# Kernel optimization log

Hardware: AMD Instinct MI355X
Metric: run time of the kernel (lower is better)

The kernel has to match this reference:

```python
import jax, jax.numpy as jnp
import numpy as np

C = 768
H = 12
HD = C // H
SCALE = HD ** -0.5
EPS = 1e-5


def setup_inputs() -> dict:
    key = jax.random.key(0)
    kit = iter(jax.random.split(key, 40))
    r = lambda *s: jax.random.normal(next(kit), s, jnp.float32) * 0.02
    d = dict(
        s_x=jax.random.normal(next(kit), (8, 196, C), jnp.float32),
        t_x=jax.random.normal(next(kit), (8, 1568, C), jnp.float32),
        ln1s_g=jnp.ones(C), ln1s_b=jnp.zeros(C),
        mha_w=r(3 * C, C), mha_b=r(3 * C), mha_ow=r(C, C), mha_ob=r(C),
        ln1t_g=jnp.ones(C), ln1t_b=jnp.zeros(C),
        attn_qkv_w=r(3 * C, C), attn_q_b=r(C), attn_v_b=r(C), attn_pw=r(C, C), attn_pb=r(C),
        lnt2s_g=jnp.ones(C), lnt2s_b=jnp.zeros(C),
        t2s_qw=r(C, C), t2s_qb=r(C), t2s_kvw=r(2 * C, C), t2s_kvb=r(C), t2s_pw=r(C, C), t2s_pb=r(C),
        lns2t_g=jnp.ones(C), lns2t_b=jnp.zeros(C),
        s2t_qw=r(C, C), s2t_qb=r(C), s2t_kvw=r(2 * C, C), s2t_kvb=r(C), s2t_pw=r(C, C), s2t_pb=r(C),
        ln2s_g=jnp.ones(C), ln2s_b=jnp.zeros(C),
        cfc_w=r(4 * C, C), cfc_b=r(4 * C), cproj_w=r(C, 4 * C), cproj_b=r(C),
        ln2t_g=jnp.ones(C), ln2t_b=jnp.zeros(C),
        fc1_w=r(4 * C, C), fc1_b=r(4 * C), fc2_w=r(C, 4 * C), fc2_b=r(C),
    )
    return d


def ln(x, g, b):
    m = x.mean(-1, keepdims=True)
    v = jnp.mean((x - m) ** 2, -1, keepdims=True)
    return (x - m) * jax.lax.rsqrt(v + EPS) * g + b


def heads(x):  # (B, N, C) -> (B, H, N, HD)
    B, N, _ = x.shape
    return x.reshape(B, N, H, HD).transpose(0, 2, 1, 3)


def mhsa(q, k, v):  # (B, H, Nq, HD), (B, H, Nk, HD) -> (B, Nq, C)
    a = jax.nn.softmax(jnp.einsum('bhqd,bhkd->bhqk', q * SCALE, k), axis=-1)
    o = jnp.einsum('bhqk,bhkd->bhqd', a, v)
    B, _, Nq, _ = o.shape
    return o.transpose(0, 2, 1, 3).reshape(B, Nq, C)


def reference(s_x, t_x, ln1s_g, ln1s_b, mha_w, mha_b, mha_ow, mha_ob,
              ln1t_g, ln1t_b, attn_qkv_w, attn_q_b, attn_v_b, attn_pw, attn_pb,
              lnt2s_g, lnt2s_b, t2s_qw, t2s_qb, t2s_kvw, t2s_kvb, t2s_pw, t2s_pb,
              lns2t_g, lns2t_b, s2t_qw, s2t_qb, s2t_kvw, s2t_kvb, s2t_pw, s2t_pb,
              ln2s_g, ln2s_b, cfc_w, cfc_b, cproj_w, cproj_b,
              ln2t_g, ln2t_b, fc1_w, fc1_b, fc2_w, fc2_b):
    # 1) clip self-attention. torch nn.MultiheadAttention (batch_first=False)
    # treats axis 0 of the (B, s_N, C) input as the sequence dim, so we
    # faithfully attend over the batch axis.
    y = ln(s_x, ln1s_g, ln1s_b)
    qkv = y @ mha_w.T + mha_b  # (B, s_N, 3C)
    q, k, v = jnp.split(qkv, 3, axis=-1)
    qt, kt, vt = (a.transpose(1, 0, 2) for a in (q, k, v))  # (s_N, B, C)
    o = mhsa(heads(qt), heads(kt), heads(vt))  # (s_N, B, C)
    o = o @ mha_ow.T + mha_ob
    s_x = s_x + o.transpose(1, 0, 2)

    # 2) video-stream self-attention (qkv_bias=True -> cat(q_b, 0, v_b))
    y = ln(t_x, ln1t_g, ln1t_b)
    qkv_bias = jnp.concatenate([attn_q_b, jnp.zeros_like(attn_v_b), attn_v_b])
    qkv = y @ attn_qkv_w.T + qkv_bias
    q, k, v = jnp.split(qkv, 3, axis=-1)
    o = mhsa(heads(q), heads(k), heads(v))
    t_x = t_x + (o @ attn_pw.T + attn_pb)

    # 3) T2S cross: query from LN(s_x), key/value from (updated, un-normed) t_x
    ys = ln(s_x, lnt2s_g, lnt2s_b)
    q = ys @ t2s_qw.T + t2s_qb
    kv = t_x @ t2s_kvw.T + jnp.concatenate([jnp.zeros_like(t2s_kvb), t2s_kvb])
    k, v = jnp.split(kv, 2, axis=-1)
    o = mhsa(heads(q), heads(k), heads(v))
    s_x = s_x + (o @ t2s_pw.T + t2s_pb)

    # 4) S2T cross: query from LN(t_x), key/value from updated s_x
    yt = ln(t_x, lns2t_g, lns2t_b)
    q = yt @ s2t_qw.T + s2t_qb
    kv = s_x @ s2t_kvw.T + jnp.concatenate([jnp.zeros_like(s2t_kvb), s2t_kvb])
    k, v = jnp.split(kv, 2, axis=-1)
    o = mhsa(heads(q), heads(k), heads(v))
    t_x = t_x + (o @ s2t_pw.T + s2t_pb)

    # 5) clip MLP (QuickGELU)
    y = ln(s_x, ln2s_g, ln2s_b)
    h = y @ cfc_w.T + cfc_b
    h = h * jax.nn.sigmoid(1.702 * h)
    s_x = s_x + (h @ cproj_w.T + cproj_b)

    # 6) video MLP (exact GELU, torch default)
    y = ln(t_x, ln2t_g, ln2t_b)
    h = jax.nn.gelu(y @ fc1_w.T + fc1_b, approximate=False)
    t_x = t_x + (h @ fc2_w.T + fc2_b)
    return (s_x, t_x)
```

## Files before the change

kernel.cpp:

```cpp
#include <hip/hip_runtime.h>
#include <stdint.h>


typedef uint16_t u16;
typedef uint16_t u16x8 __attribute__((ext_vector_type(8)));
typedef uint16_t u16x4 __attribute__((ext_vector_type(4)));
typedef short bf16x8 __attribute__((ext_vector_type(8)));
typedef float f32x4 __attribute__((ext_vector_type(4)));

__device__ __forceinline__ float b2f(u16 u) {
    union { float f; uint32_t i; } x;
    x.i = ((uint32_t)u) << 16;
    return x.f;
}
__device__ __forceinline__ u16 f2b(float f) {
    union { float f; uint32_t i; } x;
    x.f = f;
    uint32_t i = x.i;
    uint32_t r = (i + 0x7FFFu + ((i >> 16) & 1u)) >> 16;
    return (u16)r;
}
__device__ __forceinline__ u16 f2b_trunc(float f) {
    union { float f; uint32_t i; } x;
    x.f = f;
    return (u16)(x.i >> 16);
}

__device__ __forceinline__ void gload16(const u16* g, u16* l) {
    __builtin_amdgcn_global_load_lds(
        (const __attribute__((address_space(1))) uint32_t*)g,
        (__attribute__((address_space(3))) uint32_t*)l, 16, 0, 0);
}

struct CvtAll {
    const float* s[14];
    u16* d[14];
    int cum[15];
};
__global__ __launch_bounds__(256) void cvt_all(CvtAll c) {
    int i = blockIdx.x * 256 + threadIdx.x;
    if (i >= c.cum[14]) return;
    int seg = 0;
    #pragma unroll
    for (int k = 1; k < 14; k++) seg += (i >= c.cum[k]);
    int j = i - c.cum[seg];
    c.d[seg][j] = f2b(c.s[seg][j]);
}

__global__ __launch_bounds__(256) void copy_both(
    const float* __restrict__ a, const float* __restrict__ b,
    float* __restrict__ out, int na, int ntot) {
    int i = blockIdx.x * 256 + threadIdx.x;
    if (i < ntot) out[i] = (i < na) ? a[i] : b[i - na];
}

__global__ __launch_bounds__(256) void build_bias_pool(float* __restrict__ dst,
    const float* mha_b, const float* attn_q_b, const float* attn_v_b,
    const float* mha_ob, const float* attn_pb, const float* t2s_kvb,
    const float* t2s_qb, const float* t2s_pb, const float* s2t_qb,
    const float* s2t_kvb, const float* s2t_pb, const float* cfc_b,
    const float* cproj_b, const float* fc1_b, const float* fc2_b) {
    int i = blockIdx.x * 256 + threadIdx.x;
    float v = 0.f;
    if (i < 2304) v = mha_b[i];
    else if (i < 4608) { int j = i - 2304; v = (j < 768) ? attn_q_b[j] : (j < 1536 ? 0.f : attn_v_b[j - 1536]); }
    else if (i < 5376) v = mha_ob[i - 4608];
    else if (i < 6144) v = attn_pb[i - 5376];
    else if (i < 7680) { int j = i - 6144; v = (j < 768) ? 0.f : t2s_kvb[j - 768]; }
    else if (i < 8448) v = t2s_qb[i - 7680];
    else if (i < 9216) v = t2s_pb[i - 8448];
    else if (i < 9984) v = s2t_qb[i - 9216];
    else if (i < 11520) { int j = i - 9984; v = (j < 768) ? 0.f : s2t_kvb[j - 768]; }
    else if (i < 12288) v = s2t_pb[i - 11520];
    else if (i < 15360) v = cfc_b[i - 12288];
    else if (i < 16128) v = cproj_b[i - 15360];
    else if (i < 19200) v = fc1_b[i - 16128];
    else if (i < 19968) v = fc2_b[i - 19200];
    else return;
    dst[i] = v;
}

__device__ __forceinline__ float block_sum(float v, float* red) {
    #pragma unroll
    for (int o = 32; o > 0; o >>= 1) v += __shfl_down(v, o, 64);
    int w = threadIdx.x >> 6, l = threadIdx.x & 63;
    __syncthreads();
    if (l == 0) red[w] = v;
    __syncthreads();
    return red[0] + red[1] + red[2] + red[3];
}

__global__ __launch_bounds__(256) void ln_dual(
    const float* __restrict__ x, int rows0,
    const float* __restrict__ g0, const float* __restrict__ b0, u16* __restrict__ y0,
    const float* __restrict__ g1, const float* __restrict__ b1, u16* __restrict__ y1) {
    const int r = blockIdx.x;
    const int t = threadIdx.x;
    const float* g; const float* bta; u16* yr;
    if (r < rows0) { g = g0; bta = b0; yr = y0 + (size_t)r * 768; }
    else           { g = g1; bta = b1; yr = y1 + (size_t)(r - rows0) * 768; }
    const float* xr = x + (size_t)r * 768;
    float v0 = xr[t], v1 = xr[t + 256], v2 = xr[t + 512];
    __shared__ float red[4];
    float mean = block_sum(v0 + v1 + v2, red) * (1.0f / 768.0f);
    float d0 = v0 - mean, d1 = v1 - mean, d2 = v2 - mean;
    float var = block_sum(d0 * d0 + d1 * d1 + d2 * d2, red) * (1.0f / 768.0f);
    float rs = rsqrtf(var + 1e-5f);
    yr[t]       = f2b(d0 * rs * g[t]       + bta[t]);
    yr[t + 256] = f2b(d1 * rs * g[t + 256] + bta[t + 256]);
    yr[t + 512] = f2b(d2 * rs * g[t + 512] + bta[t + 512]);
}

struct TransP {
    const u16* vp; u16* vt;
    int Nk, Nkp, gx, nb;
    long long vA, vJ;
};
__device__ __forceinline__ void transpose_body(const TransP p, int bid, u16 (*T)[72]) {
    const int x = bid % p.gx, inst = bid / p.gx;
    const int a = inst / 12, h = inst % 12;
    const int t0 = x * 64;
    const int tid = threadIdx.x;
    const int kvl = tid >> 2, dseg = (tid & 3) * 16;
    u16x8 v0 = {}, v1 = {};
    if (t0 + kvl < p.Nk) {
        const u16* src = p.vp + a * p.vA + (long long)(t0 + kvl) * p.vJ + h * 64 + dseg;
        v0 = *(const u16x8*)src;
        v1 = *(const u16x8*)(src + 8);
    }
    *(u16x8*)&T[kvl][dseg]     = v0;
    *(u16x8*)&T[kvl][dseg + 8] = v1;
    __syncthreads();
    const int dl = tid >> 2, kseg = (tid & 3) * 16;
    u16x8 w0, w1;
    #pragma unroll
    for (int j = 0; j < 8; j++) w0[j] = T[kseg + j][dl];
    #pragma unroll
    for (int j = 0; j < 8; j++) w1[j] = T[kseg + 8 + j][dl];
    u16* orow = p.vt + ((size_t)inst * 64 + dl) * p.Nkp + t0 + kseg;
    *(u16x8*)orow = w0;
    *(u16x8*)(orow + 8) = w1;
}
__global__ __launch_bounds__(256) void transpose_pair(TransP p0, TransP p1) {
    __shared__ u16 T[64][72];
    int bid = blockIdx.x;
    if (bid < p0.nb) transpose_body(p0, bid, T);
    else transpose_body(p1, bid - p0.nb, T);
}

struct GemmP {
    const u16* A; const u16* W; const float* bias;
    u16* Cb; float* Cf;
    int M, N, K, gx, nb;
};
template <int MODE, int BM>
__device__ __forceinline__ void gemm_body(const GemmP p, int bid,
                                          u16 (*AsF)[32], u16 (*BsF)[32]) {
    constexpr int MI = BM / 32;
    const int tid = threadIdx.x;
    const int lane = tid & 63;
    const int wid = tid >> 6;
    const int wr = (wid >> 1) * (BM / 2), wc = (wid & 1) * 64;
    const int bx = bid % p.gx, by = bid / p.gx;
    const int m0 = bx * BM, n0 = by * 128;
    const int lr = lane >> 2, lc = (lane & 3) * 8;
    const int fr = lane & 15, fk = (lane >> 4) * 8;
    const int abase = wid * (BM / 4);
    const int bbase = wid * 32;
    f32x4 acc[MI][4] = {};
    for (int k0 = 0; k0 < p.K; k0 += 64) {
        #pragma unroll
        for (int s = 0; s < 2; s++) {
            #pragma unroll
            for (int j = 0; j < BM / 64; j++) {
                int rowa = m0 + abase + j * 16 + lr;
                rowa = rowa < p.M ? rowa : p.M - 1;
                gload16(p.A + (size_t)rowa * p.K + k0 + s * 32 + lc,
                        &AsF[s * 128 + abase + j * 16][0]);
            }
            #pragma unroll
            for (int j = 0; j < 2; j++) {
                gload16(p.W + (size_t)(n0 + bbase + j * 16 + lr) * p.K + k0 + s * 32 + lc,
                        &BsF[s * 128 + bbase + j * 16][0]);
            }
        }
        __syncthreads();
        #pragma unroll
        for (int s = 0; s < 2; s++) {
            bf16x8 a[MI], b[4];
            #pragma unroll
            for (int i = 0; i < MI; i++) a[i] = *(const bf16x8*)&AsF[s * 128 + wr + i * 16 + fr][fk];
            #pragma unroll
            for (int j = 0; j < 4; j++) b[j] = *(const bf16x8*)&BsF[s * 128 + wc + j * 16 + fr][fk];
            #pragma unroll
            for (int i = 0; i < MI; i++)
                #pragma unroll
                for (int j = 0; j < 4; j++)
                    acc[i][j] = __builtin_amdgcn_mfma_f32_16x16x32_bf16(a[i], b[j], acc[i][j], 0, 0, 0);
        }
        __syncthreads();
    }
    const int er = (lane >> 4) * 4;
    #pragma unroll
    for (int i = 0; i < MI; i++) {
        #pragma unroll
        for (int reg = 0; reg < 4; reg++) {
            int r = m0 + wr + i * 16 + er + reg;
            if (r >= p.M) continue;
            #pragma unroll
            for (int j = 0; j < 4; j++) {
                int c = n0 + wc + j * 16 + fr;
                float v = acc[i][j][reg] + p.bias[c];
                size_t idx = (size_t)r * p.N + c;
                if (MODE == 1) {
                    p.Cf[idx] += v;
                } else if (MODE == 4) {
                    float nv = p.Cf[idx] + v;
                    p.Cf[idx] = nv;
                    p.Cb[idx] = f2b(nv);
                } else {
                    if (MODE == 2) v = v / (1.0f + expf(-1.702f * v));
                    if (MODE == 3) v = 0.5f * v * (1.0f + erff(v * 0.70710678118654752f));
                    p.Cb[idx] = f2b(v);
                }
            }
        }
    }
}
template <int M0, int B0, int M1, int B1>
__global__ __launch_bounds__(256) void gemm_pair(GemmP p0, GemmP p1) {
    __shared__ u16 As[2 * 128][32];
    __shared__ u16 Bs[2 * 128][32];
    int bid = blockIdx.x;
    if (bid < p0.nb) gemm_body<M0, B0>(p0, bid, As, Bs);
    else gemm_body<M1, B1>(p1, bid - p0.nb, As, Bs);
}

struct FlashP {
    const u16* qp; const u16* kp; const u16* vt; u16* op;
    int Nq, Nk, Nkp, gx, nb;
    long long qA, qI, kA, kJ, oA, oI;
};
__device__ __forceinline__ void flash_body(const FlashP p, int bid,
    u16 (*Ks)[64][64], u16 (*Vs)[64][64], u16 (*Ps)[16][64]) {
    const int x = bid % p.gx, inst = bid / p.gx;
    const int a = inst / 12, h = inst % 12;
    const int tid = threadIdx.x, lane = tid & 63, w = tid >> 6;
    const int fr = lane & 15, g = lane >> 4, fk = g * 8;
    const int f3s = (fr & 7) << 3;
    const u16* qb = p.qp + a * p.qA + h * 64;
    const u16* kb = p.kp + a * p.kA + h * 64;
    const u16* vtb = p.vt + (size_t)inst * 64 * p.Nkp;
    const int q0 = x * 64 + w * 16;

    bf16x8 qf[2];
    {
        u16x8 raw0 = {}, raw1 = {};
        int qr = q0 + fr;
        if (qr < p.Nq) {
            const u16* qrp = qb + (long long)qr * p.qI;
            raw0 = *(const u16x8*)(qrp + fk);
            raw1 = *(const u16x8*)(qrp + 32 + fk);
        }
        const float QS = 0.125f * 1.44269504088896340736f;
        u16x8 s0, s1;
        #pragma unroll
        for (int e = 0; e < 8; e++) {
            s0[e] = f2b(b2f(raw0[e]) * QS);
            s1[e] = f2b(b2f(raw1[e]) * QS);
        }
        qf[0] = *(bf16x8*)&s0;
        qf[1] = *(bf16x8*)&s1;
    }
    float mrun = -1e30f, lrun = 0.f;
    f32x4 o[4] = {};

    const int l = lane;
    const int srow = w * 8 + (l >> 3);
    const int sdcol = ((l & 7) * 8) ^ (((l >> 3) & 7) << 3);

    auto STAGE = [&](int s, int t0) {
        #pragma unroll
        for (int c = 0; c < 2; c++) {
            int row = c * 32 + srow;
            int kr = t0 + row; if (kr >= p.Nk) kr = p.Nk - 1;
            gload16(kb + (long long)kr * p.kJ + sdcol, &Ks[s][0][0] + c * 2048 + w * 512);
            gload16(vtb + (size_t)row * p.Nkp + t0 + sdcol, &Vs[s][0][0] + c * 2048 + w * 512);
        }
    };

    const int nt = (p.Nk + 63) >> 6;
    STAGE(0, 0);
    for (int it = 0; it < nt; ++it) {
        const int t0 = it << 6;
        const int cur = it & 1;
        if (it + 1 < nt) {
            STAGE(cur ^ 1, t0 + 64);
            asm volatile("s_waitcnt vmcnt(4)" ::: "memory");
        } else {
            asm volatile("s_waitcnt vmcnt(0)" ::: "memory");
        }
        __builtin_amdgcn_s_barrier();

        f32x4 s[4] = {};
        __builtin_amdgcn_s_setprio(1);
        #pragma unroll
        for (int hh = 0; hh < 4; hh++) {
            bf16x8 k0f = *(const bf16x8*)&Ks[cur][hh * 16 + fr][fk ^ f3s];
            bf16x8 k1f = *(const bf16x8*)&Ks[cur][hh * 16 + fr][(32 + fk) ^ f3s];
            s[hh] = __builtin_amdgcn_mfma_f32_16x16x32_bf16(k0f, qf[0], s[hh], 0, 0, 0);
            s[hh] = __builtin_amdgcn_mfma_f32_16x16x32_bf16(k1f, qf[1], s[hh], 0, 0, 0);
        }
        __builtin_amdgcn_s_setprio(0);

        if (t0 + 64 > p.Nk) {
            #pragma unroll
            for (int hh = 0; hh < 4; hh++)
                #pragma unroll
                for (int r = 0; r < 4; r++)
                    if (t0 + hh * 16 + 4 * g + r >= p.Nk) s[hh][r] = -1e30f;
        }
        float a0 = fmaxf(fmaxf(s[0][0], s[0][1]), s[0][2]);
        float a1 = fmaxf(fmaxf(s[0][3], s[1][0]), s[1][1]);
        float a2 = fmaxf(fmaxf(s[1][2], s[1][3]), s[2][0]);
        float a3 = fmaxf(fmaxf(s[2][1], s[2][2]), s[2][3]);
        float a4 = fmaxf(fmaxf(s[3][0], s[3][1]), s[3][2]);
        float b0 = fmaxf(fmaxf(a0, a1), a2);
        float b1 = fmaxf(fmaxf(a3, a4), s[3][3]);
        float lmax = fmaxf(b0, b1);
        lmax = fmaxf(lmax, __shfl_xor(lmax, 16, 64));
        lmax = fmaxf(lmax, __shfl_xor(lmax, 32, 64));
        if (!__all(lmax <= mrun + 8.0f)) {
            float mn = fmaxf(mrun, lmax);
            float sf = exp2f(mrun - mn);
            mrun = mn;
            lrun *= sf;
            float sfo[4];
            #pragma unroll
            for (int r = 0; r < 4; r++) sfo[r] = __shfl(sf, g * 4 + r, 64);
            #pragma unroll
            for (int dt = 0; dt < 4; dt++)
                #pragma unroll
                for (int r = 0; r < 4; r++) o[dt][r] *= sfo[r];
        }
        float pp[4][4];
        float ps = 0.f;
        #pragma unroll
        for (int hh = 0; hh < 4; hh++)
            #pragma unroll
            for (int r = 0; r < 4; r++) {
                pp[hh][r] = exp2f(s[hh][r] - mrun);
                ps += pp[hh][r];
            }
        ps += __shfl_xor(ps, 16, 64);
        ps += __shfl_xor(ps, 32, 64);
        lrun += ps;
        #pragma unroll
        for (int hh = 0; hh < 4; hh++) {
            u16x4 pk;
            #pragma unroll
            for (int r = 0; r < 4; r++) pk[r] = f2b_trunc(pp[hh][r]);
            *(u16x4*)&Ps[w][fr][(hh * 16 + g * 4) ^ f3s] = pk;
        }
        bf16x8 pa0 = *(const bf16x8*)&Ps[w][fr][fk ^ f3s];
        bf16x8 pa1 = *(const bf16x8*)&Ps[w][fr][(32 + fk) ^ f3s];
        __builtin_amdgcn_s_setprio(1);
        #pragma unroll
        for (int dt = 0; dt < 4; dt++) {
            bf16x8 vf0 = *(const bf16x8*)&Vs[cur][dt * 16 + fr][fk ^ f3s];
            bf16x8 vf1 = *(const bf16x8*)&Vs[cur][dt * 16 + fr][(32 + fk) ^ f3s];
            o[dt] = __builtin_amdgcn_mfma_f32_16x16x32_bf16(pa0, vf0, o[dt], 0, 0, 0);
            o[dt] = __builtin_amdgcn_mfma_f32_16x16x32_bf16(pa1, vf1, o[dt], 0, 0, 0);
        }
        __builtin_amdgcn_s_setprio(0);
        __builtin_amdgcn_s_barrier();
    }
    float rcp = 1.0f / lrun;
    #pragma unroll
    for (int r = 0; r < 4; r++) {
        float rr = __shfl(rcp, g * 4 + r, 64);
        int q = q0 + g * 4 + r;
        if (q >= p.Nq) continue;
        u16* orow = p.op + a * p.oA + (long long)q * p.oI + h * 64;
        #pragma unroll
        for (int dt = 0; dt < 4; dt++)
            orow[dt * 16 + fr] = f2b(o[dt][r] * rr);
    }
}
__global__ __launch_bounds__(256) void flash_pair(FlashP p0, FlashP p1) {
    __shared__ u16 Ks[2][64][64];
    __shared__ u16 Vs[2][64][64];
    __shared__ u16 Ps[4][16][64];
    int bid = blockIdx.x;
    if (bid < p0.nb) flash_body(p0, bid, Ks, Vs, Ps);
    else flash_body(p1, bid - p0.nb, Ks, Vs, Ps);
}

extern "C" void kernel_launch(void* const* d_in, const int* in_sizes, int n_in,
                              void* d_out, int out_size, void* d_ws, size_t ws_size,
                              hipStream_t stream) {
    const int B = 8, sN = 196, tN = 1568;
    const int Ms = B * sN;
    const int Mt = B * tN;
    const int n_sf = Ms * 768;
    const int n_tf = Mt * 768;
    (void)n_in; (void)out_size; (void)ws_size;

    const bool dict_order = (in_sizes[0] == n_sf);
    auto IN = [&](int di, int ai) -> const float* {
        return (const float*)d_in[dict_order ? di : ai];
    };
    const float* in_sx      = IN(0, 35);
    const float* in_tx      = IN(1, 42);
    const float* ln1s_g     = IN(2, 14);
    const float* ln1s_b     = IN(3, 13);
    const float* mha_w      = IN(4, 28);
    const float* mha_b      = IN(5, 25);
    const float* mha_ow     = IN(6, 27);
    const float* mha_ob     = IN(7, 26);
    const float* ln1t_g     = IN(8, 16);
    const float* ln1t_b     = IN(9, 15);
    const float* attn_qkv_w = IN(10, 3);
    const float* attn_q_b   = IN(11, 2);
    const float* attn_v_b   = IN(12, 4);
    const float* attn_pw    = IN(13, 1);
    const float* attn_pb    = IN(14, 0);
    const float* lnt2s_g    = IN(15, 24);
    const float* lnt2s_b    = IN(16, 23);
    const float* t2s_qw     = IN(17, 41);
    const float* t2s_qb     = IN(18, 40);
    const float* t2s_kvw    = IN(19, 37);
    const float* t2s_kvb    = IN(20, 36);
    const float* t2s_pw     = IN(21, 39);
    const float* t2s_pb     = IN(22, 38);
    const float* lns2t_g    = IN(23, 22);
    const float* lns2t_b    = IN(24, 21);
    const float* s2t_qw     = IN(25, 34);
    const float* s2t_qb     = IN(26, 33);
    const float* s2t_kvw    = IN(27, 30);
    const float* s2t_kvb    = IN(28, 29);
    const float* s2t_pw     = IN(29, 32);
    const float* s2t_pb     = IN(30, 31);
    const float* ln2s_g     = IN(31, 18);
    const float* ln2s_b     = IN(32, 17);
    const float* cfc_w      = IN(33, 6);
    const float* cfc_b      = IN(34, 5);
    const float* cproj_w    = IN(35, 8);
    const float* cproj_b    = IN(36, 7);
    const float* ln2t_g     = IN(37, 20);
    const float* ln2t_b     = IN(38, 19);
    const float* fc1_w      = IN(39, 10);
    const float* fc1_b      = IN(40, 9);
    const float* fc2_w      = IN(41, 12);
    const float* fc2_b      = IN(42, 11);

    float* s_f = (float*)d_out;
    float* t_f = (float*)d_out + n_sf;

    char* ws = (char*)d_ws;
    size_t off = 0;
    auto take = [&](size_t bytes) { size_t o = off; off += (bytes + 255) & ~(size_t)255; return o; };
    float* biasP = (float*)(ws + take(19968 * 4));
    u16*   yb    = (u16*)(ws + take((size_t)(Ms + Mt) * 768 * 2));
    u16*   bufA  = (u16*)(ws + take((size_t)Mt * 3072 * 2));
    u16*   bufS  = (u16*)(ws + take((size_t)Mt * 768 * 2));
    u16*   bufB  = (u16*)(ws + take((size_t)Mt * 768 * 2));
    u16*   sxb   = (u16*)(ws + take((size_t)Ms * 768 * 2));
    u16*   vtb_t = (u16*)(ws + take((size_t)96 * 64 * 1600 * 2));
    u16*   yb_s  = yb;
    u16*   yb_t  = yb + (size_t)Ms * 768;
    u16*   vtb_s = yb;
    auto wtake = [&](size_t nelem) { return (u16*)(ws + take(nelem * 2)); };
    u16 *W_mha   = wtake(2304 * 768), *W_mhao  = wtake(768 * 768);
    u16 *W_qkv   = wtake(2304 * 768), *W_attnp = wtake(768 * 768);
    u16 *W_t2sq  = wtake(768 * 768),  *W_t2skv = wtake(1536 * 768), *W_t2sp = wtake(768 * 768);
    u16 *W_s2tq  = wtake(768 * 768),  *W_s2tkv = wtake(1536 * 768), *W_s2tp = wtake(768 * 768);
    u16 *W_cfc   = wtake(3072 * 768), *W_cproj = wtake(768 * 3072);
    u16 *W_fc1   = wtake(3072 * 768), *W_fc2   = wtake(768 * 3072);

    const int B_MHA = 0, B_QKV = 2304, B_MHAO = 4608, B_ATTNP = 5376;
    const int B_T2SKV = 6144, B_T2SQ = 7680, B_T2SP = 8448, B_S2TQ = 9216;
    const int B_S2TKV = 9984, B_S2TP = 11520, B_CFC = 12288, B_CPROJ = 15360;
    const int B_FC1 = 16128, B_FC2 = 19200;

    auto cdiv = [](int a, int b) { return (a + b - 1) / b; };

    {
        CvtAll c;
        const float* ss[14] = { mha_w, mha_ow, attn_qkv_w, attn_pw, t2s_qw, t2s_kvw, t2s_pw,
                                s2t_qw, s2t_kvw, s2t_pw, cfc_w, cproj_w, fc1_w, fc2_w };
        u16* dd[14] = { W_mha, W_mhao, W_qkv, W_attnp, W_t2sq, W_t2skv, W_t2sp,
                        W_s2tq, W_s2tkv, W_s2tp, W_cfc, W_cproj, W_fc1, W_fc2 };
        int nn[14] = { 2304*768, 768*768, 2304*768, 768*768, 768*768, 1536*768, 768*768,
                       768*768, 1536*768, 768*768, 3072*768, 768*3072, 3072*768, 768*3072 };
        int cum = 0;
        for (int k = 0; k < 14; k++) { c.s[k] = ss[k]; c.d[k] = dd[k]; c.cum[k] = cum; cum += nn[k]; }
        c.cum[14] = cum;
        cvt_all<<<cdiv(cum, 256), 256, 0, stream>>>(c);
    }
    build_bias_pool<<<78, 256, 0, stream>>>(biasP,
        mha_b, attn_q_b, attn_v_b, mha_ob, attn_pb, t2s_kvb, t2s_qb, t2s_pb,
        s2t_qb, s2t_kvb, s2t_pb, cfc_b, cproj_b, fc1_b, fc2_b);
    copy_both<<<cdiv(n_sf + n_tf, 256), 256, 0, stream>>>(in_sx, in_tx, s_f, n_sf, n_sf + n_tf);

    auto GP = [&](const u16* A, const u16* W, const float* bias, u16* Cb, float* Cf,
                  int M, int N, int K, int BM) {
        GemmP p; p.A = A; p.W = W; p.bias = bias; p.Cb = Cb; p.Cf = Cf;
        p.M = M; p.N = N; p.K = K; p.gx = (M + BM - 1) / BM; p.nb = p.gx * (N / 128);
        return p;
    };
    auto FP = [&](const u16* qp, const u16* kp, const u16* vt, u16* op,
                  int Nq, int Nk, int Nkp,
                  long long qA, long long qI, long long kA, long long kJ,
                  long long oA, long long oI) {
        FlashP p; p.qp = qp; p.kp = kp; p.vt = vt; p.op = op;
        p.Nq = Nq; p.Nk = Nk; p.Nkp = Nkp; p.gx = (Nq + 63) / 64;
        p.nb = p.gx * (Nq == 8 ? sN * 12 : B * 12);
        p.qA = qA; p.qI = qI; p.kA = kA; p.kJ = kJ; p.oA = oA; p.oI = oI;
        return p;
    };
    auto TP = [&](const u16* vp, u16* vt, int Nk, int Nkp, long long vA, long long vJ, int insts) {
        TransP p; p.vp = vp; p.vt = vt; p.Nk = Nk; p.Nkp = Nkp;
        p.gx = (Nk + 63) / 64; p.nb = p.gx * insts; p.vA = vA; p.vJ = vJ;
        return p;
    };

    ln_dual<<<Ms + Mt, 256, 0, stream>>>((const float*)d_out, Ms,
        ln1s_g, ln1s_b, yb_s, ln1t_g, ln1t_b, yb_t);

    {
        GemmP p0 = GP(yb_s, W_mha, biasP + B_MHA, bufS, 0, Ms, 2304, 768, 64);
        GemmP p1 = GP(yb_t, W_qkv, biasP + B_QKV, bufA, 0, Mt, 2304, 768, 128);
        gemm_pair<0, 64, 0, 128><<<p0.nb + p1.nb, 256, 0, stream>>>(p0, p1);
    }
    {
        TransP p0 = TP(bufS + 1536, vtb_s, 8, 64, 2304LL, (long long)sN * 2304, sN * 12);
        TransP p1 = TP(bufA + 1536, vtb_t, tN, 1600, (long long)tN * 2304, 2304LL, B * 12);
        transpose_pair<<<p0.nb + p1.nb, 256, 0, stream>>>(p0, p1);
    }
    {
        FlashP p0 = FP(bufS, bufS + 768, vtb_s, sxb, 8, 8, 64,
                       2304LL, (long long)sN * 2304, 2304LL, (long long)sN * 2304,
                       768LL, (long long)sN * 768);
        FlashP p1 = FP(bufA, bufA + 768, vtb_t, bufB, tN, tN, 1600,
                       (long long)tN * 2304, 2304LL, (long long)tN * 2304, 2304LL,
                       (long long)tN * 768, 768LL);
        flash_pair<<<p0.nb + p1.nb, 256, 0, stream>>>(p0, p1);
    }
    {
        GemmP p0 = GP(sxb, W_mhao, biasP + B_MHAO, 0, s_f, Ms, 768, 768, 64);
        GemmP p1 = GP(bufB, W_attnp, biasP + B_ATTNP, yb_t, t_f, Mt, 768, 768, 128);
        gemm_pair<1, 64, 4, 128><<<p0.nb + p1.nb, 256, 0, stream>>>(p0, p1);
    }
    ln_dual<<<Ms + Mt, 256, 0, stream>>>((const float*)d_out, Ms,
        lnt2s_g, lnt2s_b, yb_s, lns2t_g, lns2t_b, bufB);

    {
        GemmP p0 = GP(yb_t, W_t2skv, biasP + B_T2SKV, bufA, 0, Mt, 1536, 768, 128);
        GemmP p1 = GP(bufB, W_s2tq, biasP + B_S2TQ, bufS, 0, Mt, 768, 768, 128);
        gemm_pair<0, 128, 0, 128><<<p0.nb + p1.nb, 256, 0, stream>>>(p0, p1);
    }
    {
        TransP p0 = TP(bufA + 768, vtb_t, tN, 1600, (long long)tN * 1536, 1536LL, B * 12);
        TransP pz = p0; pz.nb = 0;
        transpose_pair<<<p0.nb, 256, 0, stream>>>(p0, pz);
    }
    {
        GemmP p0 = GP(yb_s, W_t2sq, biasP + B_T2SQ, sxb, 0, Ms, 768, 768, 64);
        GemmP pz = p0; pz.nb = 0;
        gemm_pair<0, 64, 0, 64><<<p0.nb, 256, 0, stream>>>(p0, pz);
    }
    {
        FlashP p0 = FP(sxb, bufA, vtb_t, yb_s, sN, tN, 1600,
                       (long long)sN * 768, 768LL, (long long)tN * 1536, 1536LL,
                       (long long)sN * 768, 768LL);
        FlashP pz = p0; pz.nb = 0;
        flash_pair<<<p0.nb, 256, 0, stream>>>(p0, pz);
    }
    {
        GemmP p0 = GP(yb_s, W_t2sp, biasP + B_T2SP, sxb, s_f, Ms, 768, 768, 64);
        GemmP pz = p0; pz.nb = 0;
        gemm_pair<4, 64, 4, 64><<<p0.nb, 256, 0, stream>>>(p0, pz);
    }
    {
        GemmP p0 = GP(sxb, W_s2tkv, biasP + B_S2TKV, bufB, 0, Ms, 1536, 768, 64);
        GemmP pz = p0; pz.nb = 0;
        gemm_pair<0, 64, 0, 64><<<p0.nb, 256, 0, stream>>>(p0, pz);
    }
    {
        TransP p0 = TP(bufB + 768, vtb_s, sN, 256, (long long)sN * 1536, 1536LL, B * 12);
        TransP pz = p0; pz.nb = 0;
        transpose_pair<<<p0.nb, 256, 0, stream>>>(p0, pz);
    }
    {
        FlashP p0 = FP(bufS, bufB, vtb_s, bufA, tN, sN, 256,
                       (long long)tN * 768, 768LL, (long long)sN * 1536, 1536LL,
                       (long long)tN * 768, 768LL);
        FlashP pz = p0; pz.nb = 0;
        flash_pair<<<p0.nb, 256, 0, stream>>>(p0, pz);
    }
    {
        GemmP p0 = GP(bufA, W_s2tp, biasP + B_S2TP, 0, t_f, Mt, 768, 768, 128);
        GemmP pz = p0; pz.nb = 0;
        gemm_pair<1, 128, 1, 128><<<p0.nb, 256, 0, stream>>>(p0, pz);
    }
    ln_dual<<<Ms + Mt, 256, 0, stream>>>((const float*)d_out, Ms,
        ln2s_g, ln2s_b, yb_s, ln2t_g, ln2t_b, yb_t);

    {
        GemmP p0 = GP(yb_s, W_cfc, biasP + B_CFC, bufS, 0, Ms, 3072, 768, 64);
        GemmP p1 = GP(yb_t, W_fc1, biasP + B_FC1, bufA, 0, Mt, 3072, 768, 128);
        gemm_pair<2, 64, 3, 128><<<p0.nb + p1.nb, 256, 0, stream>>>(p0, p1);
    }
    {
        GemmP p0 = GP(bufS, W_cproj, biasP + B_CPROJ, 0, s_f, Ms, 768, 3072, 64);
        GemmP p1 = GP(bufA, W_fc2, biasP + B_FC2, 0, t_f, Mt, 768, 3072, 128);
        gemm_pair<1, 64, 1, 128><<<p0.nb + p1.nb, 256, 0, stream>>>(p0, p1);
    }
}
```

Measured before the change: 968.0 us.

## Add 256x256 GEMM kernel for large video GEMMs and restructure launch schedule

Adds a 512-thread 256x256-tile GEMM with double-buffered LDS staging and XCD-aware block remapping, used for the video-token QKV, T2S KV and fc1 projections. The input copy is fused into the first layernorm, and V transposes are fused into GEMM launches. The clip MLP is reordered to run alongside the S2T KV projection, with the S2T V transpose writing into a reused buffer. These changes aim to cut launch count and raise GEMM data reuse, but they increase register/LDS pressure and reduce parallelism in some launches.

```diff
diff --git a/kernel.cpp b/kernel.cpp
--- a/kernel.cpp
+++ b/kernel.cpp
@@ -45,13 +45,6 @@
     for (int k = 1; k < 14; k++) seg += (i >= c.cum[k]);
     int j = i - c.cum[seg];
     c.d[seg][j] = f2b(c.s[seg][j]);
-}
-
-__global__ __launch_bounds__(256) void copy_both(
-    const float* __restrict__ a, const float* __restrict__ b,
-    float* __restrict__ out, int na, int ntot) {
-    int i = blockIdx.x * 256 + threadIdx.x;
-    if (i < ntot) out[i] = (i < na) ? a[i] : b[i - na];
 }
 
 __global__ __launch_bounds__(256) void build_bias_pool(float* __restrict__ dst,
@@ -90,18 +83,42 @@
     return red[0] + red[1] + red[2] + red[3];
 }
 
+__device__ __forceinline__ void ln_row(const float* xr, const float* g,
+                                       const float* bta, u16* yr, float* red) {
+    const int t = threadIdx.x;
+    float v0 = xr[t], v1 = xr[t + 256], v2 = xr[t + 512];
+    float mean = block_sum(v0 + v1 + v2, red) * (1.0f / 768.0f);
+    float d0 = v0 - mean, d1 = v1 - mean, d2 = v2 - mean;
+    float var = block_sum(d0 * d0 + d1 * d1 + d2 * d2, red) * (1.0f / 768.0f);
+    float rs = rsqrtf(var + 1e-5f);
+    yr[t]       = f2b(d0 * rs * g[t]       + bta[t]);
+    yr[t + 256] = f2b(d1 * rs * g[t + 256] + bta[t + 256]);
+    yr[t + 512] = f2b(d2 * rs * g[t + 512] + bta[t + 512]);
+}
+
 __global__ __launch_bounds__(256) void ln_dual(
     const float* __restrict__ x, int rows0,
-    const float* __restrict__ g0, const float* __restrict__ b0, u16* __restrict__ y0,
-    const float* __restrict__ g1, const float* __restrict__ b1, u16* __restrict__ y1) {
-    const int r = blockIdx.x;
-    const int t = threadIdx.x;
-    const float* g; const float* bta; u16* yr;
-    if (r < rows0) { g = g0; bta = b0; yr = y0 + (size_t)r * 768; }
-    else           { g = g1; bta = b1; yr = y1 + (size_t)(r - rows0) * 768; }
-    const float* xr = x + (size_t)r * 768;
+    const float* g0, const float* b0, u16* y0,
+    const float* g1, const float* b1, u16* y1) {
+    __shared__ float red[4];
+    int r = blockIdx.x;
+    if (r < rows0) ln_row(x + (size_t)r * 768, g0, b0, y0 + (size_t)r * 768, red);
+    else ln_row(x + (size_t)r * 768, g1, b1, y1 + (size_t)(r - rows0) * 768, red);
+}
+
+__global__ __launch_bounds__(256) void ln_dual_in(
+    const float* __restrict__ xs, const float* __restrict__ xt,
+    float* __restrict__ xcopy, int rows0,
+    const float* g0, const float* b0, u16* y0,
+    const float* g1, const float* b1, u16* y1) {
+    __shared__ float red[4];
+    int r = blockIdx.x, t = threadIdx.x;
+    const float* xr; const float* g; const float* bta; u16* yr;
+    if (r < rows0) { xr = xs + (size_t)r * 768; g = g0; bta = b0; yr = y0 + (size_t)r * 768; }
+    else { xr = xt + (size_t)(r - rows0) * 768; g = g1; bta = b1; yr = y1 + (size_t)(r - rows0) * 768; }
     float v0 = xr[t], v1 = xr[t + 256], v2 = xr[t + 512];
-    __shared__ float red[4];
+    float* xc = xcopy + (size_t)r * 768;
+    xc[t] = v0; xc[t + 256] = v1; xc[t + 512] = v2;
     float mean = block_sum(v0 + v1 + v2, red) * (1.0f / 768.0f);
     float d0 = v0 - mean, d1 = v1 - mean, d2 = v2 - mean;
     float var = block_sum(d0 * d0 + d1 * d1 + d2 * d2, red) * (1.0f / 768.0f);
@@ -235,6 +252,141 @@
     if (bid < p0.nb) gemm_body<M0, B0>(p0, bid, As, Bs);
     else gemm_body<M1, B1>(p1, bid - p0.nb, As, Bs);
 }
+template <int M0, int B0, int M1, int B1>
+__global__ __launch_bounds__(256) void gemm2_trans(GemmP p0, GemmP p1, TransP t0) {
+    __shared__ u16 As[2 * 128][32];
+    __shared__ u16 Bs[2 * 128][32];
+    int bid = blockIdx.x;
+    if (bid < p0.nb) gemm_body<M0, B0>(p0, bid, As, Bs);
+    else if (bid < p0.nb + p1.nb) gemm_body<M1, B1>(p1, bid - p0.nb, As, Bs);
+    else transpose_body(t0, bid - p0.nb - p1.nb, (u16(*)[72])&As[0][0]);
+}
+
+template <int MODE>
+__global__ __launch_bounds__(512) void gemm256(
+    const u16* __restrict__ A, const u16* __restrict__ W,
+    const float* __restrict__ bias, u16* __restrict__ Cb,
+    float* __restrict__ Cf, int M, int N, int K) {
+    __shared__ u16 LA[2][256][64];
+    __shared__ u16 LB[2][256][64];
+    const int tid = threadIdx.x;
+    const int lane = tid & 63, wid = tid >> 6;
+    const int wm = wid >> 2, wn = wid & 3;
+    int nwg = gridDim.x;
+    int q = nwg >> 3, r8 = nwg & 7;
+    int xcd = blockIdx.x & 7, orig = blockIdx.x >> 3;
+    int bid = (xcd < r8 ? xcd * (q + 1) : r8 * (q + 1) + (xcd - r8) * q) + orig;
+    const int gx = M >> 8;
+    const int bx = bid % gx, by = bid / gx;
+    const int m0 = bx * 256, n0 = by * 256;
+    const int srow = tid >> 3;
+    const int sgcol = ((tid & 7) * 8) ^ (((tid >> 3) & 7) << 3);
+    const u16* Ag = A + (size_t)m0 * K;
+    const u16* Bg = W + (size_t)n0 * K;
+    const int fr = lane & 15, g = lane >> 4, fk = g * 8;
+    const int rsw = (fr & 7) << 3;
+
+    auto stageHalf = [&](u16* half, const u16* gsrc, int rowOff, int kc) {
+        #pragma unroll
+        for (int c = 0; c < 2; c++) {
+            int row = rowOff + c * 64 + srow;
+            gload16(gsrc + (size_t)row * K + kc + sgcol,
+                    half + c * 4096 + wid * 512);
+        }
+    };
+    auto stage1 = [&](int s, int kc, int which) {
+        if (which == 0) stageHalf(&LB[s][0][0],   Bg, 0,   kc);
+        else if (which == 1) stageHalf(&LB[s][128][0], Bg, 128, kc);
+        else if (which == 2) stageHalf(&LA[s][0][0],   Ag, 0,   kc);
+        else stageHalf(&LA[s][128][0], Ag, 128, kc);
+    };
+
+    f32x4 acc[8][4] = {};
+    const int NT = K >> 6;
+    stage1(0, 0, 0); stage1(0, 0, 1); stage1(0, 0, 2); stage1(0, 0, 3);
+
+    for (int kt = 0; kt < NT; kt++) {
+        const int cur = kt & 1;
+        const int kn = (kt + 1) << 6;
+        const bool pf = (kt + 1 < NT);
+        asm volatile("s_waitcnt vmcnt(2)" ::: "memory");
+        __builtin_amdgcn_s_barrier();
+        bf16x8 bfr[4][2];
+        #pragma unroll
+        for (int fj = 0; fj < 4; fj++)
+            #pragma unroll
+            for (int ks = 0; ks < 2; ks++)
+                bfr[fj][ks] = *(const bf16x8*)&LB[cur][wn * 64 + fj * 16 + fr][(ks * 32 + fk) ^ rsw];
+        #pragma unroll
+        for (int ph = 0; ph < 2; ph++) {
+            bf16x8 afr[2][2];
+            #pragma unroll
+            for (int i2 = 0; i2 < 2; i2++)
+                #pragma unroll
+                for (int ks = 0; ks < 2; ks++)
+                    afr[i2][ks] = *(const bf16x8*)&LA[cur][(ph * 2 + i2) * 32 + wm * 16 + fr][(ks * 32 + fk) ^ rsw];
+            if (pf) stage1(cur ^ 1, kn, ph);
+            __builtin_amdgcn_s_setprio(1);
+            #pragma unroll
+            for (int i2 = 0; i2 < 2; i2++)
+                #pragma unroll
+                for (int ks = 0; ks < 2; ks++)
+                    #pragma unroll
+                    for (int fj = 0; fj < 4; fj++)
+                        acc[ph * 2 + i2][fj] = __builtin_amdgcn_mfma_f32_16x16x32_bf16(
+                            afr[i2][ks], bfr[fj][ks], acc[ph * 2 + i2][fj], 0, 0, 0);
+            __builtin_amdgcn_s_setprio(0);
+        }
+        if (pf) asm volatile("s_waitcnt vmcnt(4)" ::: "memory");
+        else    asm volatile("s_waitcnt vmcnt(0)" ::: "memory");
+        __builtin_amdgcn_s_barrier();
+        #pragma unroll
+        for (int ph = 2; ph < 4; ph++) {
+            bf16x8 afr[2][2];
+            #pragma unroll
+            for (int i2 = 0; i2 < 2; i2++)
+                #pragma unroll
+                for (int ks = 0; ks < 2; ks++)
+                    afr[i2][ks] = *(const bf16x8*)&LA[cur][(ph * 2 + i2) * 32 + wm * 16 + fr][(ks * 32 + fk) ^ rsw];
+            if (pf) stage1(cur ^ 1, kn, ph);
+            __builtin_amdgcn_s_setprio(1);
+            #pragma unroll
+            for (int i2 = 0; i2 < 2; i2++)
+                #pragma unroll
+                for (int ks = 0; ks < 2; ks++)
+                    #pragma unroll
+                    for (int fj = 0; fj < 4; fj++)
+                        acc[ph * 2 + i2][fj] = __builtin_amdgcn_mfma_f32_16x16x32_bf16(
+                            afr[i2][ks], bfr[fj][ks], acc[ph * 2 + i2][fj], 0, 0, 0);
+            __builtin_amdgcn_s_setprio(0);
+        }
+    }
+    const int er = g * 4;
+    #pragma unroll
+    for (int fi = 0; fi < 8; fi++) {
+        #pragma unroll
+        for (int reg = 0; reg < 4; reg++) {
+            int rr = m0 + fi * 32 + wm * 16 + er + reg;
+            #pragma unroll
+            for (int fj = 0; fj < 4; fj++) {
+                int c = n0 + wn * 64 + fj * 16 + fr;
+                float v = acc[fi][fj][reg] + bias[c];
+                size_t idx = (size_t)rr * N + c;
+                if (MODE == 1) {
+                    Cf[idx] += v;
+                } else if (MODE == 4) {
+                    float nv = Cf[idx] + v;
+                    Cf[idx] = nv;
+                    Cb[idx] = f2b(nv);
+                } else {
+                    if (MODE == 2) v = v / (1.0f + expf(-1.702f * v));
+                    if (MODE == 3) v = 0.5f * v * (1.0f + erff(v * 0.70710678118654752f));
+                    Cb[idx] = f2b(v);
+                }
+            }
+        }
+    }
+}
 
 struct FlashP {
     const u16* qp; const u16* kp; const u16* vt; u16* op;
@@ -379,9 +531,9 @@
     #pragma unroll
     for (int r = 0; r < 4; r++) {
         float rr = __shfl(rcp, g * 4 + r, 64);
-        int q = q0 + g * 4 + r;
-        if (q >= p.Nq) continue;
-        u16* orow = p.op + a * p.oA + (long long)q * p.oI + h * 64;
+        int qq = q0 + g * 4 + r;
+        if (qq >= p.Nq) continue;
+        u16* orow = p.op + a * p.oA + (long long)qq * p.oI + h * 64;
         #pragma unroll
         for (int dt = 0; dt < 4; dt++)
             orow[dt * 16 + fr] = f2b(o[dt][r] * rr);
@@ -501,7 +653,6 @@
     build_bias_pool<<<78, 256, 0, stream>>>(biasP,
         mha_b, attn_q_b, attn_v_b, mha_ob, attn_pb, t2s_kvb, t2s_qb, t2s_pb,
         s2t_qb, s2t_kvb, s2t_pb, cfc_b, cproj_b, fc1_b, fc2_b);
-    copy_both<<<cdiv(n_sf + n_tf, 256), 256, 0, stream>>>(in_sx, in_tx, s_f, n_sf, n_sf + n_tf);
 
     auto GP = [&](const u16* A, const u16* W, const float* bias, u16* Cb, float* Cf,
                   int M, int N, int K, int BM) {
@@ -509,13 +660,13 @@
         p.M = M; p.N = N; p.K = K; p.gx = (M + BM - 1) / BM; p.nb = p.gx * (N / 128);
         return p;
     };
-    auto FP = [&](const u16* qp, const u16* kp, const u16* vt, u16* op,
-                  int Nq, int Nk, int Nkp,
-                  long long qA, long long qI, long long kA, long long kJ,
-                  long long oA, long long oI) {
+    auto FPm = [&](const u16* qp, const u16* kp, const u16* vt, u16* op,
+                   int Nq, int Nk, int Nkp, int insts,
+                   long long qA, long long qI, long long kA, long long kJ,
+                   long long oA, long long oI) {
         FlashP p; p.qp = qp; p.kp = kp; p.vt = vt; p.op = op;
         p.Nq = Nq; p.Nk = Nk; p.Nkp = Nkp; p.gx = (Nq + 63) / 64;
-        p.nb = p.gx * (Nq == 8 ? sN * 12 : B * 12);
+        p.nb = p.gx * insts;
         p.qA = qA; p.qI = qI; p.kA = kA; p.kJ = kJ; p.oA = oA; p.oI = oI;
         return p;
     };
@@ -525,13 +676,14 @@
         return p;
     };
 
-    ln_dual<<<Ms + Mt, 256, 0, stream>>>((const float*)d_out, Ms,
+    ln_dual_in<<<Ms + Mt, 256, 0, stream>>>(in_sx, in_tx, (float*)d_out, Ms,
         ln1s_g, ln1s_b, yb_s, ln1t_g, ln1t_b, yb_t);
 
+    gemm256<0><<<49 * (2304 / 256), 512, 0, stream>>>(yb_t, W_qkv, biasP + B_QKV, bufA, (float*)0, Mt, 2304, 768);
     {
         GemmP p0 = GP(yb_s, W_mha, biasP + B_MHA, bufS, 0, Ms, 2304, 768, 64);
-        GemmP p1 = GP(yb_t, W_qkv, biasP + B_QKV, bufA, 0, Mt, 2304, 768, 128);
-        gemm_pair<0, 64, 0, 128><<<p0.nb + p1.nb, 256, 0, stream>>>(p0, p1);
+        GemmP pz = p0; pz.nb = 0;
+        gemm_pair<0, 64, 0, 64><<<p0.nb, 256, 0, stream>>>(p0, pz);
     }
     {
         TransP p0 = TP(bufS + 1536, vtb_s, 8, 64, 2304LL, (long long)sN * 2304, sN * 12);
@@ -539,12 +691,12 @@
         transpose_pair<<<p0.nb + p1.nb, 256, 0, stream>>>(p0, p1);
     }
     {
-        FlashP p0 = FP(bufS, bufS + 768, vtb_s, sxb, 8, 8, 64,
-                       2304LL, (long long)sN * 2304, 2304LL, (long long)sN * 2304,
-                       768LL, (long long)sN * 768);
-        FlashP p1 = FP(bufA, bufA + 768, vtb_t, bufB, tN, tN, 1600,
-                       (long long)tN * 2304, 2304LL, (long long)tN * 2304, 2304LL,
-                       (long long)tN * 768, 768LL);
+        FlashP p0 = FPm(bufS, bufS + 768, vtb_s, sxb, 8, 8, 64, sN * 12,
+                        2304LL, (long long)sN * 2304, 2304LL, (long long)sN * 2304,
+                        768LL, (long long)sN * 768);
+        FlashP p1 = FPm(bufA, bufA + 768, vtb_t, bufB, tN, tN, 1600, B * 12,
+                        (long long)tN * 2304, 2304LL, (long long)tN * 2304, 2304LL,
+                        (long long)tN * 768, 768LL);
         flash_pair<<<p0.nb + p1.nb, 256, 0, stream>>>(p0, p1);
     }
     {
@@ -554,26 +706,17 @@
     }
     ln_dual<<<Ms + Mt, 256, 0, stream>>>((const float*)d_out, Ms,
         lnt2s_g, lnt2s_b, yb_s, lns2t_g, lns2t_b, bufB);
-
-    {
-        GemmP p0 = GP(yb_t, W_t2skv, biasP + B_T2SKV, bufA, 0, Mt, 1536, 768, 128);
-        GemmP p1 = GP(bufB, W_s2tq, biasP + B_S2TQ, bufS, 0, Mt, 768, 768, 128);
-        gemm_pair<0, 128, 0, 128><<<p0.nb + p1.nb, 256, 0, stream>>>(p0, p1);
-    }
-    {
-        TransP p0 = TP(bufA + 768, vtb_t, tN, 1600, (long long)tN * 1536, 1536LL, B * 12);
-        TransP pz = p0; pz.nb = 0;
-        transpose_pair<<<p0.nb, 256, 0, stream>>>(p0, pz);
-    }
-    {
-        GemmP p0 = GP(yb_s, W_t2sq, biasP + B_T2SQ, sxb, 0, Ms, 768, 768, 64);
-        GemmP pz = p0; pz.nb = 0;
-        gemm_pair<0, 64, 0, 64><<<p0.nb, 256, 0, stream>>>(p0, pz);
-    }
-    {
-        FlashP p0 = FP(sxb, bufA, vtb_t, yb_s, sN, tN, 1600,
-                       (long long)sN * 768, 768LL, (long long)tN * 1536, 1536LL,
-                       (long long)sN * 768, 768LL);
+    gemm256<0><<<49 * (1536 / 256), 512, 0, stream>>>(yb_t, W_t2skv, biasP + B_T2SKV, bufA, (float*)0, Mt, 1536, 768);
+    {
+        GemmP p0 = GP(bufB, W_s2tq, biasP + B_S2TQ, bufS, 0, Mt, 768, 768, 128);
+        GemmP p1 = GP(yb_s, W_t2sq, biasP + B_T2SQ, sxb, 0, Ms, 768, 768, 64);
+        TransP t0 = TP(bufA + 768, vtb_t, tN, 1600, (long long)tN * 1536, 1536LL, B * 12);
+        gemm2_trans<0, 128, 0, 64><<<p0.nb + p1.nb + t0.nb, 256, 0, stream>>>(p0, p1, t0);
+    }
+    {
+        FlashP p0 = FPm(sxb, bufA, vtb_t, yb_s, sN, tN, 1600, B * 12,
+                        (long long)sN * 768, 768LL, (long long)tN * 1536, 1536LL,
+                        (long long)sN * 768, 768LL);
         FlashP pz = p0; pz.nb = 0;
         flash_pair<<<p0.nb, 256, 0, stream>>>(p0, pz);
     }
@@ -582,39 +725,37 @@
         GemmP pz = p0; pz.nb = 0;
         gemm_pair<4, 64, 4, 64><<<p0.nb, 256, 0, stream>>>(p0, pz);
     }
+    ln_dual<<<Ms, 256, 0, stream>>>((const float*)d_out, Ms,
+        ln2s_g, ln2s_b, yb_s, ln2s_g, ln2s_b, yb_s);
     {
         GemmP p0 = GP(sxb, W_s2tkv, biasP + B_S2TKV, bufB, 0, Ms, 1536, 768, 64);
+        GemmP p1 = GP(yb_s, W_cfc, biasP + B_CFC, yb_t, 0, Ms, 3072, 768, 64);
+        gemm_pair<0, 64, 2, 64><<<p0.nb + p1.nb, 256, 0, stream>>>(p0, p1);
+    }
+    {
+        GemmP p0 = GP(yb_t, W_cproj, biasP + B_CPROJ, 0, s_f, Ms, 768, 3072, 64);
         GemmP pz = p0; pz.nb = 0;
-        gemm_pair<0, 64, 0, 64><<<p0.nb, 256, 0, stream>>>(p0, pz);
-    }
-    {
-        TransP p0 = TP(bufB + 768, vtb_s, sN, 256, (long long)sN * 1536, 1536LL, B * 12);
-        TransP pz = p0; pz.nb = 0;
-        transpose_pair<<<p0.nb, 256, 0, stream>>>(p0, pz);
-    }
-    {
-        FlashP p0 = FP(bufS, bufB, vtb_s, bufA, tN, sN, 256,
-                       (long long)tN * 768, 768LL, (long long)sN * 1536, 1536LL,
-                       (long long)tN * 768, 768LL);
+        TransP t0 = TP(bufB + 768, bufA, sN, 256, (long long)sN * 1536, 1536LL, B * 12);
+        gemm2_trans<1, 64, 1, 64><<<p0.nb + t0.nb, 256, 0, stream>>>(p0, pz, t0);
+    }
+    {
+        FlashP p0 = FPm(bufS, bufB, bufA, yb, tN, sN, 256, B * 12,
+                        (long long)tN * 768, 768LL, (long long)sN * 1536, 1536LL,
+                        (long long)tN * 768, 768LL);
         FlashP pz = p0; pz.nb = 0;
         flash_pair<<<p0.nb, 256, 0, stream>>>(p0, pz);
     }
     {
-        GemmP p0 = GP(bufA, W_s2tp, biasP + B_S2TP, 0, t_f, Mt, 768, 768, 128);
+        GemmP p0 = GP(yb, W_s2tp, biasP + B_S2TP, 0, t_f, Mt, 768, 768, 128);
         GemmP pz = p0; pz.nb = 0;
         gemm_pair<1, 128, 1, 128><<<p0.nb, 256, 0, stream>>>(p0, pz);
     }
-    ln_dual<<<Ms + Mt, 256, 0, stream>>>((const float*)d_out, Ms,
-        ln2s_g, ln2s_b, yb_s, ln2t_g, ln2t_b, yb_t);
-
-    {
-        GemmP p0 = GP(yb_s, W_cfc, biasP + B_CFC, bufS, 0, Ms, 3072, 768, 64);
-        GemmP p1 = GP(yb_t, W_fc1, biasP + B_FC1, bufA, 0, Mt, 3072, 768, 128);
-        gemm_pair<2, 64, 3, 128><<<p0.nb + p1.nb, 256, 0, stream>>>(p0, p1);
-    }
-    {
-        GemmP p0 = GP(bufS, W_cproj, biasP + B_CPROJ, 0, s_f, Ms, 768, 3072, 64);
-        GemmP p1 = GP(bufA, W_fc2, biasP + B_FC2, 0, t_f, Mt, 768, 3072, 128);
-        gemm_pair<1, 64, 1, 128><<<p0.nb + p1.nb, 256, 0, stream>>>(p0, p1);
-    }
-}
+    ln_dual<<<Mt, 256, 0, stream>>>(t_f, 0,
+        ln2t_g, ln2t_b, yb_t, ln2t_g, ln2t_b, yb_t);
+    gemm256<3><<<49 * (3072 / 256), 512, 0, stream>>>(yb_t, W_fc1, biasP + B_FC1, bufA, (float*)0, Mt, 3072, 768);
+    {
+        GemmP p0 = GP(bufA, W_fc2, biasP + B_FC2, 0, t_f, Mt, 768, 3072, 128);
+        GemmP pz = p0; pz.nb = 0;
+        gemm_pair<1, 128, 1, 128><<<p0.nb, 256, 0, stream>>>(p0, pz);
+    }
+}
```

Result: faster. 929.6 us (-4.0%).
